# Kernel optimization log

Hardware: AMD Instinct MI355X
Metric: run time of the kernel (lower is better)

The kernel has to match this reference:

```python
import jax, jax.numpy as jnp
import numpy as np

B, T1, CHUNK = 4, 512, 64
LEFT, RIGHT = 256, 64
T2 = T1 + LEFT + RIGHT          # 832
NPOS = 2 * T1 - 1 + LEFT + RIGHT  # 1343
NFEAT, H, DK = 1024, 16, 64


def setup_inputs() -> dict:
    key = jax.random.key(0)
    ks = jax.random.split(key, 14)
    s = 0.02
    inp = {
        "query":   jax.random.normal(ks[0], (B, T1, NFEAT), jnp.float32),
        "key":     jax.random.normal(ks[1], (B, T2, NFEAT), jnp.float32),
        "value":   jax.random.normal(ks[2], (B, T2, NFEAT), jnp.float32),
        "pos_emb": jax.random.normal(ks[3], (1, NPOS, NFEAT), jnp.float32),
        "Wq":   jax.random.normal(ks[4], (NFEAT, NFEAT), jnp.float32) * s,
        "bq":   jax.random.normal(ks[5], (NFEAT,), jnp.float32) * s,
        "Wk":   jax.random.normal(ks[6], (NFEAT, NFEAT), jnp.float32) * s,
        "bk":   jax.random.normal(ks[7], (NFEAT,), jnp.float32) * s,
        "Wv":   jax.random.normal(ks[8], (NFEAT, NFEAT), jnp.float32) * s,
        "bv":   jax.random.normal(ks[9], (NFEAT,), jnp.float32) * s,
        "Wpos": jax.random.normal(ks[10], (NFEAT, NFEAT), jnp.float32) * s,
        "Wout": jax.random.normal(ks[11], (NFEAT, NFEAT), jnp.float32) * s,
        "bout": jax.random.normal(ks[12], (NFEAT,), jnp.float32) * s,
        "pos_bias_u": jax.random.normal(ks[13], (H, DK), jnp.float32) * s,
        "pos_bias_v": jax.random.normal(jax.random.fold_in(key, 99), (H, DK), jnp.float32) * s,
    }
    # chunk mask with right context: key index j maps to absolute position a = j - LEFT;
    # query i (chunk c = i // CHUNK) may attend a in [c*CHUNK - LEFT, (c+1)*CHUNK + RIGHT)
    c = np.arange(T1) // CHUNK
    a = np.arange(T2) - LEFT
    allowed = (a[None, :] < (c[:, None] + 1) * CHUNK + RIGHT) & (a[None, :] >= c[:, None] * CHUNK - LEFT)
    inp["mask"] = jnp.broadcast_to(jnp.asarray(allowed, dtype=bool)[None], (B, T1, T2))
    inp["left_context_size"] = LEFT
    inp["right_context_size"] = RIGHT
    return inp


def _rel_shift(x, left, right):
    # x: (b, h, t1, 2*t1-1+left+right) -> (b, h, t1, t1+left+right)
    # matches torch as_strided: out[..., i, j] = x[..., i, j - i + t1 - 1]
    b, h, t1, n = x.shape
    t2 = t1 + left + right
    idx = jnp.arange(t2)[None, :] - jnp.arange(t1)[:, None] + (t1 - 1)  # (t1, t2)
    return jnp.take_along_axis(x, idx[None, None], axis=-1)


def reference(query, key, value, pos_emb, mask, Wq, bq, Wk, bk, Wv, bv,
              Wpos, Wout, bout, pos_bias_u, pos_bias_v,
              left_context_size, right_context_size):
    b, t1, _ = query.shape
    q = (query @ Wq.T + bq).reshape(b, t1, H, DK)                       # (b, t1, h, d)
    k = (key @ Wk.T + bk).reshape(b, -1, H, DK).transpose(0, 2, 1, 3)    # (b, h, t2, d)
    v = (value @ Wv.T + bv).reshape(b, -1, H, DK).transpose(0, 2, 1, 3)  # (b, h, t2, d)
    p = (pos_emb @ Wpos.T).reshape(pos_emb.shape[0], -1, H, DK).transpose(0, 2, 1, 3)  # (1, h, n, d)

    q_u = (q + pos_bias_u).transpose(0, 2, 1, 3)   # (b, h, t1, d)
    q_v = (q + pos_bias_v).transpose(0, 2, 1, 3)   # (b, h, t1, d)

    matrix_ac = jnp.einsum('bhqd,bhkd->bhqk', q_u, k)          # (b, h, t1, t2)
    matrix_bd = jnp.einsum('bhqd,ohnd->bhqn', q_v, p)          # (b, h, t1, n)
    matrix_bd = _rel_shift(matrix_bd, left_context_size, right_context_size)

    scores = (matrix_ac + matrix_bd) / jnp.sqrt(jnp.float32(DK))
    m = mask[:, None, :, :]                                    # (b, 1, t1, t2), True = attend
    scores = jnp.where(m, scores, -jnp.inf)
    attn = jax.nn.softmax(scores.astype(jnp.float32), axis=-1).astype(value.dtype)
    attn = jnp.where(m, attn, 0.0)

    x = jnp.einsum('bhqk,bhkd->bqhd', attn, v).reshape(b, t1, H * DK)
    out = x @ Wout.T + bout                                     # (b, t1, n_feat)
    new_cache = jnp.concatenate([k, v], axis=-1)                # (b, h, t2, 2*d)
    return out, new_cache
```

## Files before the change

### kernel.cpp

```cpp
#include <hip/hip_runtime.h>
#include <cstdint>

typedef unsigned short u16;
using short8 = __attribute__((ext_vector_type(8))) short;
using f32x4  = __attribute__((ext_vector_type(4))) float;

#define T1 512
#define T2 832
#define NH 16
#define NPLOC 448

__device__ __forceinline__ u16 f2b(float f){
  union { float f; uint32_t u; } c; c.f = f;
  uint32_t u = c.u;
  u += 0x7fffu + ((u >> 16) & 1u);
  return (u16)(u >> 16);
}
__device__ __forceinline__ float b2f(u16 b){
  union { uint32_t u; float f; } c; c.u = (uint32_t)b << 16; return c.f;
}
__device__ __forceinline__ void async16(const void* g, void* l){
  __builtin_amdgcn_global_load_lds(
      (const __attribute__((address_space(1))) unsigned int*)g,
      (__attribute__((address_space(3))) unsigned int*)l, 16, 0, 0);
}

struct CvtSeg { const float* src; u16* dst; int nblk; };
struct CvtArgs { CvtSeg s[9]; };

__global__ __launch_bounds__(256) void cvt_all(CvtArgs a){
  int rel = blockIdx.x, seg = 0;
  while (rel >= a.s[seg].nblk){ rel -= a.s[seg].nblk; ++seg; }
  int i = rel * 256 + threadIdx.x;
  float4 v = ((const float4*)a.s[seg].src)[i];
  uint64_t p = (uint64_t)f2b(v.x) | ((uint64_t)f2b(v.y) << 16)
             | ((uint64_t)f2b(v.z) << 32) | ((uint64_t)f2b(v.w) << 48);
  *(uint64_t*)(a.s[seg].dst + (size_t)i * 4) = p;
}

__device__ __forceinline__ void gemm_core128(const u16* __restrict__ A, const u16* __restrict__ W,
    int m0, int n0, int tid, f32x4 acc[4][4])
{
  __shared__ __align__(16) u16 As0[4096];
  __shared__ __align__(16) u16 As1[4096];
  __shared__ __align__(16) u16 Bs0[4096];
  __shared__ __align__(16) u16 Bs1[4096];

  int lane = tid & 63, w = tid >> 6;
  int wr = w >> 1, wc = w & 1;
  const int lr = lane & 15, g = lane >> 4;
  const int sslot = (g ^ ((lr >> 1) & 3)) * 8;

  int r = tid >> 2;
  int ssl = ((tid & 3) ^ ((tid >> 3) & 3)) * 8;
  const u16* Asrc = A + (size_t)(m0 + r) * 1024 + ssl;
  const u16* Bsrc = W + (size_t)(n0 + r) * 1024 + ssl;

  auto stage = [&](int k0, u16* as, u16* bs){
    async16(Asrc + k0,         as + tid*8);
    async16(Asrc + 65536 + k0, as + 2048 + tid*8);
    async16(Bsrc + k0,         bs + tid*8);
    async16(Bsrc + 65536 + k0, bs + 2048 + tid*8);
  };

  auto step = [&](u16* as, u16* bs, int kstage, bool do_stage, bool last){
    if (last) asm volatile("s_waitcnt vmcnt(0)" ::: "memory");
    else      asm volatile("s_waitcnt vmcnt(4)" ::: "memory");
    __builtin_amdgcn_sched_barrier(0);
    __builtin_amdgcn_s_barrier();
    __builtin_amdgcn_sched_barrier(0);
    short8 a[4], b[4];
    #pragma unroll
    for (int m = 0; m < 4; ++m) a[m] = *(const short8*)&as[(wr*64 + m*16 + lr)*32 + sslot];
    #pragma unroll
    for (int n = 0; n < 4; ++n) b[n] = *(const short8*)&bs[(wc*64 + n*16 + lr)*32 + sslot];
    asm volatile("s_waitcnt lgkmcnt(0)" ::: "memory");
    __builtin_amdgcn_sched_barrier(0);
    __builtin_amdgcn_s_barrier();
    __builtin_amdgcn_sched_barrier(0);
    if (do_stage) stage(kstage, as, bs);
    __builtin_amdgcn_sched_barrier(0);
    __builtin_amdgcn_s_setprio(1);
    #pragma unroll
    for (int m = 0; m < 4; ++m)
      #pragma unroll
      for (int n = 0; n < 4; ++n)
        acc[m][n] = __builtin_amdgcn_mfma_f32_16x16x32_bf16(a[m], b[n], acc[m][n], 0, 0, 0);
    __builtin_amdgcn_s_setprio(0);
  };

  stage(0,  As0, Bs0);
  stage(32, As1, Bs1);
  __builtin_amdgcn_sched_barrier(0);
  for (int it = 0; it < 16; ++it){
    step(As0, Bs0, it*64 + 64, it < 15, false);
    step(As1, Bs1, it*64 + 96, it < 15, it == 15);
  }
}

__device__ __forceinline__ void gemm_core64(const u16* __restrict__ A, const u16* __restrict__ W,
    int m0, int n0, int tid, f32x4 acc[4][2])
{
  __shared__ __align__(16) u16 As0[2048];
  __shared__ __align__(16) u16 As1[2048];
  __shared__ __align__(16) u16 Bs0[4096];
  __shared__ __align__(16) u16 Bs1[4096];

  int lane = tid & 63, wc = tid >> 6;
  const int lr = lane & 15, g = lane >> 4;
  const int sslot = (g ^ ((lr >> 1) & 3)) * 8;

  int r = tid >> 2;
  int ssl = ((tid & 3) ^ ((tid >> 3) & 3)) * 8;
  const u16* Asrc = A + (size_t)(m0 + r) * 1024 + ssl;
  const u16* Bsrc = W + (size_t)(n0 + r) * 1024 + ssl;

  auto stage = [&](int k0, u16* as, u16* bs){
    async16(Asrc + k0,         as + tid*8);
    async16(Bsrc + k0,         bs + tid*8);
    async16(Bsrc + 65536 + k0, bs + 2048 + tid*8);
  };

  auto step = [&](u16* as, u16* bs, int kstage, bool do_stage, bool last){
    if (last) asm volatile("s_waitcnt vmcnt(0)" ::: "memory");
    else      asm volatile("s_waitcnt vmcnt(3)" ::: "memory");
    __builtin_amdgcn_sched_barrier(0);
    __builtin_amdgcn_s_barrier();
    __builtin_amdgcn_sched_barrier(0);
    short8 a[4], b[2];
    #pragma unroll
    for (int m = 0; m < 4; ++m) a[m] = *(const short8*)&as[(m*16 + lr)*32 + sslot];
    #pragma unroll
    for (int n = 0; n < 2; ++n) b[n] = *(const short8*)&bs[(wc*32 + n*16 + lr)*32 + sslot];
    asm volatile("s_waitcnt lgkmcnt(0)" ::: "memory");
    __builtin_amdgcn_sched_barrier(0);
    __builtin_amdgcn_s_barrier();
    __builtin_amdgcn_sched_barrier(0);
    if (do_stage) stage(kstage, as, bs);
    __builtin_amdgcn_sched_barrier(0);
    __builtin_amdgcn_s_setprio(1);
    #pragma unroll
    for (int m = 0; m < 4; ++m)
      #pragma unroll
      for (int n = 0; n < 2; ++n)
        acc[m][n] = __builtin_amdgcn_mfma_f32_16x16x32_bf16(a[m], b[n], acc[m][n], 0, 0, 0);
    __builtin_amdgcn_s_setprio(0);
  };

  stage(0,  As0, Bs0);
  stage(32, As1, Bs1);
  __builtin_amdgcn_sched_barrier(0);
  for (int it = 0; it < 16; ++it){
    step(As0, Bs0, it*64 + 64, it < 15, false);
    step(As1, Bs1, it*64 + 96, it < 15, it == 15);
  }
}

struct G4Args {
  const u16 *q, *k, *v, *p;
  const u16 *Wq, *Wk, *Wv, *Wp;
  const float *bq, *bk, *bv, *pbu, *pbv;
  u16 *qu, *qv2, *katt, *vatt, *patt;
  float *cache;
};

__global__ __launch_bounds__(256, 4) void gemm4(G4Args ga){
  int bid0 = blockIdx.x;
  int bid = (bid0 & 7) * 72 + (bid0 >> 3);
  int tid = threadIdx.x;
  int mode, mb; const u16 *A, *W;
  if (bid < 128)      { mode = 0; mb = bid >> 3;         A = ga.q; W = ga.Wq; }
  else if (bid < 336) { mode = 1; mb = (bid - 128) >> 3; A = ga.k; W = ga.Wk; }
  else if (bid < 544) { mode = 2; mb = (bid - 336) >> 3; A = ga.v; W = ga.Wv; }
  else                { mode = 3; mb = (bid - 544) >> 3; A = ga.p; W = ga.Wp; }
  int m0 = mb * 128, n0 = (bid & 7) * 128;
  f32x4 acc[4][4] = {};
  gemm_core128(A, W, m0, n0, tid, acc);

  int lane = tid & 63, w = tid >> 6;
  int wr = w >> 1, wc = w & 1;
  const int lr = lane & 15, g = lane >> 4;
  #pragma unroll
  for (int m = 0; m < 4; ++m){
    #pragma unroll
    for (int n = 0; n < 4; ++n){
      #pragma unroll
      for (int j = 0; j < 4; ++j){
        int row = m0 + wr*64 + m*16 + g*4 + j;
        int col = n0 + wc*64 + n*16 + lr;
        float vv = acc[m][n][j];
        if (mode == 0){
          vv += ga.bq[col];
          int h = col >> 6, d = col & 63, b_ = row >> 9, t = row & 511;
          size_t o = ((size_t)((b_*NH + h)*T1 + t))*64 + d;
          ga.qu [o] = f2b(vv + ga.pbu[col]);
          ga.qv2[o] = f2b(vv + ga.pbv[col]);
        } else if (mode == 1 || mode == 2){
          vv += (mode == 1 ? ga.bk : ga.bv)[col];
          int h = col >> 6, d = col & 63;
          int b_ = row / T2, t2 = row - b_*T2;
          size_t base = (size_t)(b_*NH + h)*T2 + t2;
          ga.cache[base*128 + (mode == 2 ? 64 : 0) + d] = vv;
          (mode == 1 ? ga.katt : ga.vatt)[base*64 + d] = f2b(vv);
        } else {
          if (row < NPLOC){
            int h = col >> 6, d = col & 63;
            ga.patt[((size_t)h*NPLOC + row)*64 + d] = f2b(vv);
          }
        }
      }
    }
  }
}

__global__ __launch_bounds__(256, 4) void gemm_out(const u16* __restrict__ A, const u16* __restrict__ W,
                                                   const float* __restrict__ bias, float* __restrict__ out){
  int bid0 = blockIdx.x;
  int bid = (bid0 & 7) * 32 + (bid0 >> 3);
  int m0 = (bid >> 3) * 64, n0 = (bid & 7) * 128;
  int tid = threadIdx.x;
  f32x4 acc[4][2] = {};
  gemm_core64(A, W, m0, n0, tid, acc);
  int lane = tid & 63, wc = tid >> 6;
  const int lr = lane & 15, g = lane >> 4;
  #pragma unroll
  for (int m = 0; m < 4; ++m)
    #pragma unroll
    for (int n = 0; n < 2; ++n)
      #pragma unroll
      for (int j = 0; j < 4; ++j){
        int row = m0 + m*16 + g*4 + j;
        int col = n0 + wc*32 + n*16 + lr;
        out[(size_t)row*1024 + col] = acc[m][n][j] + bias[col];
      }
}

#define PHASE_HEAD(N) \
  asm volatile("s_waitcnt vmcnt(" #N ")" ::: "memory"); \
  __builtin_amdgcn_sched_barrier(0); \
  __builtin_amdgcn_s_barrier(); \
  __builtin_amdgcn_sched_barrier(0);

#define PHASE_TAIL \
  __builtin_amdgcn_sched_barrier(0); \
  __builtin_amdgcn_s_barrier(); \
  __builtin_amdgcn_sched_barrier(0);

#define VT_TAIL \
  asm volatile("s_waitcnt lgkmcnt(0)" ::: "memory"); \
  __builtin_amdgcn_sched_barrier(0); \
  __builtin_amdgcn_s_barrier(); \
  __builtin_amdgcn_sched_barrier(0);

__global__ __launch_bounds__(256, 2) void attn_v3(
    const u16* __restrict__ qu, const u16* __restrict__ qv,
    const u16* __restrict__ katt, const u16* __restrict__ vatt,
    const u16* __restrict__ patt, u16* __restrict__ xout)
{
  __shared__ __align__(16) u16 SB[64*384];
  __shared__ __align__(16) u16 S0[8192];
  __shared__ __align__(16) u16 S1[8192];

  int tid = threadIdx.x, lane = tid & 63, w = tid >> 6;
  int bid0 = blockIdx.x;
  int bid = (bid0 & 7) * 64 + (bid0 >> 3);
  int c = bid & 7, h = (bid >> 3) & 15, b = bid >> 7;
  int bh = b*NH + h;
  const int lr = lane & 15, g = lane >> 4, lk = g * 8;

  auto sb_off = [&](int r, int cc) -> uint32_t {
    return ((uint32_t)(r*384 + cc)*2) ^ ((uint32_t)(r & 15) << 4);
  };
  auto stg_swz = [&](uint32_t o) -> uint32_t { return o ^ (((o >> 7) & 7u) << 4); };
  auto vt_off = [&](int d, int kk) -> uint32_t {
    return ((uint32_t)(d*128 + kk)*2) ^ ((uint32_t)(((d & 7) ^ ((d >> 3) & 7))) << 4);
  };

  int qrow = 16*w + lr;
  const u16* qub = qu + ((size_t)bh*T1 + c*64 + qrow)*64;
  const u16* qvb = qv + ((size_t)bh*T1 + c*64 + qrow)*64;
  short8 qu0 = *(const short8*)(qub + lk);
  short8 qu1 = *(const short8*)(qub + 32 + lk);
  short8 qv0 = *(const short8*)(qvb + lk);
  short8 qv1 = *(const short8*)(qvb + 32 + lk);
  __builtin_amdgcn_sched_barrier(0);

  const char* psrc = (const char*)(patt + (size_t)h*NPLOC*64);
  const char* ksrc = (const char*)(katt + ((size_t)bh*T2 + c*64)*64);
  const u16*  vsrc = vatt + ((size_t)bh*T2 + c*64)*64;

  auto issue4 = [&](const char* src, u16* dst){
    #pragma unroll
    for (int i = 0; i < 4; ++i){
      uint32_t o = (uint32_t)(i*256 + tid)*16;
      async16(src + stg_swz(o), (char*)dst + o);
    }
  };

  uint4 vstg0, vstg1, vstg2, vstg3;
  auto vload = [&](int vc){
    const u16* vb = vsrc + vc*8192;
    vstg0 = *(const uint4*)(vb + (0*256 + tid)*8);
    vstg1 = *(const uint4*)(vb + (1*256 + tid)*8);
    vstg2 = *(const uint4*)(vb + (2*256 + tid)*8);
    vstg3 = *(const uint4*)(vb + (3*256 + tid)*8);
  };
  auto vtwrite = [&](u16* sbuf){
    #pragma unroll
    for (int i = 0; i < 4; ++i){
      uint4 vv4 = (i == 0) ? vstg0 : (i == 1) ? vstg1 : (i == 2) ? vstg2 : vstg3;
      int e = (i*256 + tid)*8;
      int kk = e >> 6, d0 = e & 63;
      u16 uu[8] = { (u16)(vv4.x & 0xffff), (u16)(vv4.x >> 16), (u16)(vv4.y & 0xffff), (u16)(vv4.y >> 16),
                    (u16)(vv4.z & 0xffff), (u16)(vv4.z >> 16), (u16)(vv4.w & 0xffff), (u16)(vv4.w >> 16) };
      #pragma unroll
      for (int j = 0; j < 8; ++j)
        *(u16*)((char*)sbuf + vt_off(d0 + j, kk)) = uu[j];
    }
  };

  #define BD_CHUNK(PC, SBUF) \
    _Pragma("unroll") \
    for (int nt = 0; nt < 8; ++nt){ \
      uint32_t bo = (uint32_t)((nt*16 + lr)*64)*2; \
      short8 b0 = *(const short8*)((const char*)SBUF + stg_swz(bo + lk*2)); \
      short8 b1 = *(const short8*)((const char*)SBUF + stg_swz(bo + (32 + lk)*2)); \
      f32x4 acc = {0.f,0.f,0.f,0.f}; \
      __builtin_amdgcn_s_setprio(1); \
      acc = __builtin_amdgcn_mfma_f32_16x16x32_bf16(qv0, b0, acc, 0, 0, 0); \
      acc = __builtin_amdgcn_mfma_f32_16x16x32_bf16(qv1, b1, acc, 0, 0, 0); \
      __builtin_amdgcn_s_setprio(0); \
      int nl = (PC)*128 + nt*16 + lr; \
      _Pragma("unroll") \
      for (int j = 0; j < 4; ++j){ \
        int r = 16*w + g*4 + j; \
        int jj = nl + r - 63; \
        if (jj >= 0 && jj < 384) *(u16*)((char*)SB + sb_off(r, jj)) = f2b(acc[j]); \
      } \
    }

  #define AC_CHUNK(KC, SBUF) \
    _Pragma("unroll") \
    for (int nt = 0; nt < 8; ++nt){ \
      uint32_t bo = (uint32_t)((nt*16 + lr)*64)*2; \
      short8 b0 = *(const short8*)((const char*)SBUF + stg_swz(bo + lk*2)); \
      short8 b1 = *(const short8*)((const char*)SBUF + stg_swz(bo + (32 + lk)*2)); \
      __builtin_amdgcn_s_setprio(1); \
      accs[(KC)*8 + nt] = __builtin_amdgcn_mfma_f32_16x16x32_bf16(qu0, b0, accs[(KC)*8 + nt], 0, 0, 0); \
      accs[(KC)*8 + nt] = __builtin_amdgcn_mfma_f32_16x16x32_bf16(qu1, b1, accs[(KC)*8 + nt], 0, 0, 0); \
      __builtin_amdgcn_s_setprio(0); \
    }

  #define PV_CHUNK(VC, SBUF) \
    _Pragma("unroll") \
    for (int kt = 0; kt < 4; ++kt){ \
      short8 a = *(const short8*)((const char*)SB + sb_off(16*w + lr, (VC)*128 + kt*32 + lk)); \
      __builtin_amdgcn_s_setprio(1); \
      _Pragma("unroll") \
      for (int n = 0; n < 4; ++n){ \
        short8 bb = *(const short8*)((const char*)SBUF + vt_off(n*16 + lr, kt*32 + lk)); \
        acco[n] = __builtin_amdgcn_mfma_f32_16x16x32_bf16(a, bb, acco[n], 0, 0, 0); \
      } \
      __builtin_amdgcn_s_setprio(0); \
    }

  f32x4 accs[24];
  #pragma unroll
  for (int t = 0; t < 24; ++t) accs[t] = (f32x4){0.f,0.f,0.f,0.f};
  f32x4 acco[4] = {};

  issue4(psrc,          S0);
  issue4(psrc + 16384,  S1);

  PHASE_HEAD(4) BD_CHUNK(0, S0) PHASE_TAIL issue4(psrc + 32768, S0);
  PHASE_HEAD(4) BD_CHUNK(1, S1) PHASE_TAIL issue4(psrc + 49152, S1);
  PHASE_HEAD(4) BD_CHUNK(2, S0) PHASE_TAIL issue4(ksrc,         S0);
  PHASE_HEAD(4) BD_CHUNK(3, S1) PHASE_TAIL issue4(ksrc + 16384, S1);
  PHASE_HEAD(4) AC_CHUNK(0, S0) PHASE_TAIL issue4(ksrc + 32768, S0);
  PHASE_HEAD(4) AC_CHUNK(1, S1) PHASE_TAIL vload(0);
  PHASE_HEAD(4) AC_CHUNK(2, S0)

  #pragma unroll
  for (int t = 0; t < 24; ++t)
    #pragma unroll
    for (int j = 0; j < 4; ++j){
      int r = 16*w + g*4 + j, cc = t*16 + lr;
      accs[t][j] += b2f(*(const u16*)((const char*)SB + sb_off(r, cc)));
    }
  float mx[4] = {-1e30f,-1e30f,-1e30f,-1e30f};
  #pragma unroll
  for (int t = 0; t < 24; ++t)
    #pragma unroll
    for (int j = 0; j < 4; ++j) mx[j] = fmaxf(mx[j], accs[t][j]);
  #pragma unroll
  for (int j = 0; j < 4; ++j){
    mx[j] = fmaxf(mx[j], __shfl_xor(mx[j], 1));
    mx[j] = fmaxf(mx[j], __shfl_xor(mx[j], 2));
    mx[j] = fmaxf(mx[j], __shfl_xor(mx[j], 4));
    mx[j] = fmaxf(mx[j], __shfl_xor(mx[j], 8));
  }
  float sm[4] = {0.f,0.f,0.f,0.f};
  #pragma unroll
  for (int t = 0; t < 24; ++t)
    #pragma unroll
    for (int j = 0; j < 4; ++j){
      accs[t][j] = __expf((accs[t][j] - mx[j]) * 0.125f);
      sm[j] += accs[t][j];
    }
  #pragma unroll
  for (int j = 0; j < 4; ++j){
    sm[j] += __shfl_xor(sm[j], 1);
    sm[j] += __shfl_xor(sm[j], 2);
    sm[j] += __shfl_xor(sm[j], 4);
    sm[j] += __shfl_xor(sm[j], 8);
    sm[j] = 1.f / sm[j];
  }
  #pragma unroll
  for (int t = 0; t < 24; ++t)
    #pragma unroll
    for (int j = 0; j < 4; ++j){
      int r = 16*w + g*4 + j, cc = t*16 + lr;
      *(u16*)((char*)SB + sb_off(r, cc)) = f2b(accs[t][j] * sm[j]);
    }

  asm volatile("s_waitcnt vmcnt(0)" ::: "memory");
  __builtin_amdgcn_sched_barrier(0);
  vtwrite(S1);
  vload(1);
  VT_TAIL

  PV_CHUNK(0, S1)
  asm volatile("s_waitcnt vmcnt(0)" ::: "memory");
  __builtin_amdgcn_sched_barrier(0);
  vtwrite(S0);
  vload(2);
  VT_TAIL

  PV_CHUNK(1, S0)
  asm volatile("s_waitcnt vmcnt(0)" ::: "memory");
  __builtin_amdgcn_sched_barrier(0);
  vtwrite(S1);
  VT_TAIL

  PV_CHUNK(2, S1)

  #pragma unroll
  for (int n = 0; n < 4; ++n)
    #pragma unroll
    for (int j = 0; j < 4; ++j){
      int r = 16*w + g*4 + j;
      int t = c*64 + r, d = n*16 + lr;
      xout[((size_t)b*T1 + t)*1024 + h*64 + d] = f2b(acco[n][j]);
    }
}

extern "C" void kernel_launch(void* const* d_in, const int* in_sizes, int n_in,
                              void* d_out, int out_size, void* d_ws, size_t ws_size,
                              hipStream_t stream)
{
  const float* query = (const float*)d_in[0];
  const float* key   = (const float*)d_in[1];
  const float* value = (const float*)d_in[2];
  const float* pos   = (const float*)d_in[3];
  const float* Wq  = (const float*)d_in[4];
  const float* bq  = (const float*)d_in[5];
  const float* Wk  = (const float*)d_in[6];
  const float* bk  = (const float*)d_in[7];
  const float* Wv  = (const float*)d_in[8];
  const float* bv  = (const float*)d_in[9];
  const float* Wp  = (const float*)d_in[10];
  const float* Wo  = (const float*)d_in[11];
  const float* bo  = (const float*)d_in[12];
  const float* pbu = (const float*)d_in[13];
  const float* pbv = (const float*)d_in[14];

  float* out   = (float*)d_out;
  float* cache = out + 2097152;

  u16* ws     = (u16*)d_ws;
  u16* q_bf   = ws;
  u16* key_bf = ws + 2097152;
  u16* val_bf = ws + 5505024;
  u16* pos_bf = ws + 8912896;
  u16* Wq_bf  = ws + 9437184;
  u16* Wk_bf  = ws + 10485760;
  u16* Wv_bf  = ws + 11534336;
  u16* Wp_bf  = ws + 12582912;
  u16* Wo_bf  = ws + 13631488;
  u16* qu_bf  = ws + 14680064;
  u16* qv_bf  = ws + 16777216;
  u16* katt   = ws + 18874368;
  u16* vatt   = ws + 22282240;
  u16* patt   = ws + 25690112;
  u16* x_bf   = ws + 26148864;

  CvtArgs ca;
  ca.s[0] = { query,            q_bf,   2048 };
  ca.s[1] = { key,              key_bf, 3328 };
  ca.s[2] = { value,            val_bf, 3328 };
  ca.s[3] = { Wq,               Wq_bf,  1024 };
  ca.s[4] = { Wk,               Wk_bf,  1024 };
  ca.s[5] = { Wv,               Wv_bf,  1024 };
  ca.s[6] = { Wp,               Wp_bf,  1024 };
  ca.s[7] = { Wo,               Wo_bf,  1024 };
  ca.s[8] = { pos + 448*1024,   pos_bf, 448 };
  cvt_all<<<14272, 256, 0, stream>>>(ca);

  G4Args ga;
  ga.q = q_bf; ga.k = key_bf; ga.v = val_bf; ga.p = pos_bf;
  ga.Wq = Wq_bf; ga.Wk = Wk_bf; ga.Wv = Wv_bf; ga.Wp = Wp_bf;
  ga.bq = bq; ga.bk = bk; ga.bv = bv; ga.pbu = pbu; ga.pbv = pbv;
  ga.qu = qu_bf; ga.qv2 = qv_bf; ga.katt = katt; ga.vatt = vatt; ga.patt = patt;
  ga.cache = cache;
  gemm4<<<576, 256, 0, stream>>>(ga);

  attn_v3<<<512, 256, 0, stream>>>(qu_bf, qv_bf, katt, vatt, patt, x_bf);

  gemm_out<<<256, 256, 0, stream>>>(x_bf, Wo_bf, bo, out);
}
```

Measured before the change: 89.84 us.

## Fuse fp32-to-bf16 activation conversion into projection GEMM A-tile loads

The projection GEMM now reads the fp32 query/key/value/pos activations directly into registers, converts them to bf16 and writes them to LDS. This replaces the async global-to-LDS copies from a pre-converted buffer, so the separate conversion pass now only handles the weights. It removes the extra write and re-read of the bf16 activation buffers, but the GEMM loads twice as many bytes of A per tile, uses more registers (occupancy bound lowered from 4 to 3), and does conversion ALU work inside the main loop.

```diff
diff --git a/kernel.cpp b/kernel.cpp
--- a/kernel.cpp
+++ b/kernel.cpp
@@ -25,8 +25,10 @@
       (__attribute__((address_space(3))) unsigned int*)l, 16, 0, 0);
 }
 
+#define SB0 __builtin_amdgcn_sched_barrier(0)
+
 struct CvtSeg { const float* src; u16* dst; int nblk; };
-struct CvtArgs { CvtSeg s[9]; };
+struct CvtArgs { CvtSeg s[5]; };
 
 __global__ __launch_bounds__(256) void cvt_all(CvtArgs a){
   int rel = blockIdx.x, seg = 0;
@@ -38,148 +40,103 @@
   *(uint64_t*)(a.s[seg].dst + (size_t)i * 4) = p;
 }
 
-__device__ __forceinline__ void gemm_core128(const u16* __restrict__ A, const u16* __restrict__ W,
-    int m0, int n0, int tid, f32x4 acc[4][4])
-{
-  __shared__ __align__(16) u16 As0[4096];
-  __shared__ __align__(16) u16 As1[4096];
-  __shared__ __align__(16) u16 Bs0[4096];
-  __shared__ __align__(16) u16 Bs1[4096];
-
-  int lane = tid & 63, w = tid >> 6;
-  int wr = w >> 1, wc = w & 1;
-  const int lr = lane & 15, g = lane >> 4;
-  const int sslot = (g ^ ((lr >> 1) & 3)) * 8;
-
-  int r = tid >> 2;
-  int ssl = ((tid & 3) ^ ((tid >> 3) & 3)) * 8;
-  const u16* Asrc = A + (size_t)(m0 + r) * 1024 + ssl;
-  const u16* Bsrc = W + (size_t)(n0 + r) * 1024 + ssl;
-
-  auto stage = [&](int k0, u16* as, u16* bs){
-    async16(Asrc + k0,         as + tid*8);
-    async16(Asrc + 65536 + k0, as + 2048 + tid*8);
-    async16(Bsrc + k0,         bs + tid*8);
-    async16(Bsrc + 65536 + k0, bs + 2048 + tid*8);
-  };
-
-  auto step = [&](u16* as, u16* bs, int kstage, bool do_stage, bool last){
-    if (last) asm volatile("s_waitcnt vmcnt(0)" ::: "memory");
-    else      asm volatile("s_waitcnt vmcnt(4)" ::: "memory");
-    __builtin_amdgcn_sched_barrier(0);
-    __builtin_amdgcn_s_barrier();
-    __builtin_amdgcn_sched_barrier(0);
-    short8 a[4], b[4];
-    #pragma unroll
-    for (int m = 0; m < 4; ++m) a[m] = *(const short8*)&as[(wr*64 + m*16 + lr)*32 + sslot];
-    #pragma unroll
-    for (int n = 0; n < 4; ++n) b[n] = *(const short8*)&bs[(wc*64 + n*16 + lr)*32 + sslot];
-    asm volatile("s_waitcnt lgkmcnt(0)" ::: "memory");
-    __builtin_amdgcn_sched_barrier(0);
-    __builtin_amdgcn_s_barrier();
-    __builtin_amdgcn_sched_barrier(0);
-    if (do_stage) stage(kstage, as, bs);
-    __builtin_amdgcn_sched_barrier(0);
-    __builtin_amdgcn_s_setprio(1);
-    #pragma unroll
-    for (int m = 0; m < 4; ++m)
-      #pragma unroll
-      for (int n = 0; n < 4; ++n)
-        acc[m][n] = __builtin_amdgcn_mfma_f32_16x16x32_bf16(a[m], b[n], acc[m][n], 0, 0, 0);
-    __builtin_amdgcn_s_setprio(0);
-  };
-
-  stage(0,  As0, Bs0);
-  stage(32, As1, Bs1);
-  __builtin_amdgcn_sched_barrier(0);
-  for (int it = 0; it < 16; ++it){
-    step(As0, Bs0, it*64 + 64, it < 15, false);
-    step(As1, Bs1, it*64 + 96, it < 15, it == 15);
-  }
-}
-
-__device__ __forceinline__ void gemm_core64(const u16* __restrict__ A, const u16* __restrict__ W,
-    int m0, int n0, int tid, f32x4 acc[4][2])
-{
-  __shared__ __align__(16) u16 As0[2048];
-  __shared__ __align__(16) u16 As1[2048];
-  __shared__ __align__(16) u16 Bs0[4096];
-  __shared__ __align__(16) u16 Bs1[4096];
-
-  int lane = tid & 63, wc = tid >> 6;
-  const int lr = lane & 15, g = lane >> 4;
-  const int sslot = (g ^ ((lr >> 1) & 3)) * 8;
-
-  int r = tid >> 2;
-  int ssl = ((tid & 3) ^ ((tid >> 3) & 3)) * 8;
-  const u16* Asrc = A + (size_t)(m0 + r) * 1024 + ssl;
-  const u16* Bsrc = W + (size_t)(n0 + r) * 1024 + ssl;
-
-  auto stage = [&](int k0, u16* as, u16* bs){
-    async16(Asrc + k0,         as + tid*8);
-    async16(Bsrc + k0,         bs + tid*8);
-    async16(Bsrc + 65536 + k0, bs + 2048 + tid*8);
-  };
-
-  auto step = [&](u16* as, u16* bs, int kstage, bool do_stage, bool last){
-    if (last) asm volatile("s_waitcnt vmcnt(0)" ::: "memory");
-    else      asm volatile("s_waitcnt vmcnt(3)" ::: "memory");
-    __builtin_amdgcn_sched_barrier(0);
-    __builtin_amdgcn_s_barrier();
-    __builtin_amdgcn_sched_barrier(0);
-    short8 a[4], b[2];
-    #pragma unroll
-    for (int m = 0; m < 4; ++m) a[m] = *(const short8*)&as[(m*16 + lr)*32 + sslot];
-    #pragma unroll
-    for (int n = 0; n < 2; ++n) b[n] = *(const short8*)&bs[(wc*32 + n*16 + lr)*32 + sslot];
-    asm volatile("s_waitcnt lgkmcnt(0)" ::: "memory");
-    __builtin_amdgcn_sched_barrier(0);
-    __builtin_amdgcn_s_barrier();
-    __builtin_amdgcn_sched_barrier(0);
-    if (do_stage) stage(kstage, as, bs);
-    __builtin_amdgcn_sched_barrier(0);
-    __builtin_amdgcn_s_setprio(1);
-    #pragma unroll
-    for (int m = 0; m < 4; ++m)
-      #pragma unroll
-      for (int n = 0; n < 2; ++n)
-        acc[m][n] = __builtin_amdgcn_mfma_f32_16x16x32_bf16(a[m], b[n], acc[m][n], 0, 0, 0);
-    __builtin_amdgcn_s_setprio(0);
-  };
-
-  stage(0,  As0, Bs0);
-  stage(32, As1, Bs1);
-  __builtin_amdgcn_sched_barrier(0);
-  for (int it = 0; it < 16; ++it){
-    step(As0, Bs0, it*64 + 64, it < 15, false);
-    step(As1, Bs1, it*64 + 96, it < 15, it == 15);
-  }
-}
-
 struct G4Args {
-  const u16 *q, *k, *v, *p;
+  const float *q, *k, *v, *p;
   const u16 *Wq, *Wk, *Wv, *Wp;
   const float *bq, *bk, *bv, *pbu, *pbv;
   u16 *qu, *qv2, *katt, *vatt, *patt;
   float *cache;
 };
 
-__global__ __launch_bounds__(256, 4) void gemm4(G4Args ga){
+__global__ __launch_bounds__(256, 3) void gemm4(G4Args ga){
+  __shared__ __align__(16) u16 As0[4096];
+  __shared__ __align__(16) u16 As1[4096];
+  __shared__ __align__(16) u16 Bs0[4096];
+  __shared__ __align__(16) u16 Bs1[4096];
+
   int bid0 = blockIdx.x;
   int bid = (bid0 & 7) * 72 + (bid0 >> 3);
   int tid = threadIdx.x;
-  int mode, mb; const u16 *A, *W;
+  int mode, mb; const float *A; const u16 *W;
   if (bid < 128)      { mode = 0; mb = bid >> 3;         A = ga.q; W = ga.Wq; }
   else if (bid < 336) { mode = 1; mb = (bid - 128) >> 3; A = ga.k; W = ga.Wk; }
   else if (bid < 544) { mode = 2; mb = (bid - 336) >> 3; A = ga.v; W = ga.Wv; }
   else                { mode = 3; mb = (bid - 544) >> 3; A = ga.p; W = ga.Wp; }
   int m0 = mb * 128, n0 = (bid & 7) * 128;
-  f32x4 acc[4][4] = {};
-  gemm_core128(A, W, m0, n0, tid, acc);
 
   int lane = tid & 63, w = tid >> 6;
   int wr = w >> 1, wc = w & 1;
   const int lr = lane & 15, g = lane >> 4;
+  const int sslot = (g ^ ((lr >> 1) & 3)) * 8;
+
+  int r = tid >> 2;
+  int ssl = ((tid & 3) ^ ((tid >> 3) & 3)) * 8;
+  const float* Af  = A + (size_t)(m0 + r) * 1024 + ssl;
+  const u16*  Bsrc = W + (size_t)(n0 + r) * 1024 + ssl;
+
+  f32x4 acc[4][4] = {};
+  float4 xA0, xA1, xA2, xA3, yA0, yA1, yA2, yA3;
+
+#define LOADX(K) { xA0 = *(const float4*)(Af+(K)); xA1 = *(const float4*)(Af+(K)+4); \
+                   xA2 = *(const float4*)(Af+(K)+65536); xA3 = *(const float4*)(Af+(K)+65536+4); }
+#define LOADY(K) { yA0 = *(const float4*)(Af+(K)); yA1 = *(const float4*)(Af+(K)+4); \
+                   yA2 = *(const float4*)(Af+(K)+65536); yA3 = *(const float4*)(Af+(K)+65536+4); }
+#define WRX(AS) { short8 p0, p1; \
+  p0[0]=(short)f2b(xA0.x); p0[1]=(short)f2b(xA0.y); p0[2]=(short)f2b(xA0.z); p0[3]=(short)f2b(xA0.w); \
+  p0[4]=(short)f2b(xA1.x); p0[5]=(short)f2b(xA1.y); p0[6]=(short)f2b(xA1.z); p0[7]=(short)f2b(xA1.w); \
+  p1[0]=(short)f2b(xA2.x); p1[1]=(short)f2b(xA2.y); p1[2]=(short)f2b(xA2.z); p1[3]=(short)f2b(xA2.w); \
+  p1[4]=(short)f2b(xA3.x); p1[5]=(short)f2b(xA3.y); p1[6]=(short)f2b(xA3.z); p1[7]=(short)f2b(xA3.w); \
+  *(short8*)((AS) + tid*8) = p0; *(short8*)((AS) + 2048 + tid*8) = p1; }
+#define WRY(AS) { short8 p0, p1; \
+  p0[0]=(short)f2b(yA0.x); p0[1]=(short)f2b(yA0.y); p0[2]=(short)f2b(yA0.z); p0[3]=(short)f2b(yA0.w); \
+  p0[4]=(short)f2b(yA1.x); p0[5]=(short)f2b(yA1.y); p0[6]=(short)f2b(yA1.z); p0[7]=(short)f2b(yA1.w); \
+  p1[0]=(short)f2b(yA2.x); p1[1]=(short)f2b(yA2.y); p1[2]=(short)f2b(yA2.z); p1[3]=(short)f2b(yA2.w); \
+  p1[4]=(short)f2b(yA3.x); p1[5]=(short)f2b(yA3.y); p1[6]=(short)f2b(yA3.z); p1[7]=(short)f2b(yA3.w); \
+  *(short8*)((AS) + tid*8) = p0; *(short8*)((AS) + 2048 + tid*8) = p1; }
+#define ISSUEB(BS, K) { async16(Bsrc + (K), (BS) + tid*8); \
+                        async16(Bsrc + 65536 + (K), (BS) + 2048 + tid*8); }
+
+#define GSTEP(AS, BS, TOPW, DW, WRM, LDM, KA, KB, IA, IB) { \
+  asm volatile("s_waitcnt vmcnt(" #TOPW ")" ::: "memory"); \
+  SB0; __builtin_amdgcn_s_barrier(); SB0; \
+  short8 a_[4], b_[4]; \
+  _Pragma("unroll") \
+  for (int m = 0; m < 4; ++m) a_[m] = *(const short8*)&(AS)[(wr*64 + m*16 + lr)*32 + sslot]; \
+  _Pragma("unroll") \
+  for (int n = 0; n < 4; ++n) b_[n] = *(const short8*)&(BS)[(wc*64 + n*16 + lr)*32 + sslot]; \
+  asm volatile("s_waitcnt lgkmcnt(0)" ::: "memory"); \
+  SB0; __builtin_amdgcn_s_barrier(); SB0; \
+  if (DW){ asm volatile("s_waitcnt vmcnt(2)" ::: "memory"); SB0; WRM(AS); } \
+  if (IA){ LDM(KA); } \
+  if (IB){ ISSUEB(BS, KB); } \
+  SB0; \
+  __builtin_amdgcn_s_setprio(1); \
+  _Pragma("unroll") \
+  for (int m = 0; m < 4; ++m) \
+    _Pragma("unroll") \
+    for (int n = 0; n < 4; ++n) \
+      acc[m][n] = __builtin_amdgcn_mfma_f32_16x16x32_bf16(a_[m], b_[n], acc[m][n], 0, 0, 0); \
+  __builtin_amdgcn_s_setprio(0); }
+
+  LOADX(0);
+  ISSUEB(Bs0, 0);
+  LOADY(32);
+  asm volatile("s_waitcnt vmcnt(6)" ::: "memory"); SB0;
+  WRX(As0);
+  LOADX(64);
+  ISSUEB(Bs1, 32);
+  asm volatile("s_waitcnt vmcnt(6)" ::: "memory"); SB0;
+  WRY(As1);
+  asm volatile("s_waitcnt lgkmcnt(0)" ::: "memory"); SB0;
+
+  for (int it = 0; it < 15; ++it){
+    int t0 = 2*it;
+    GSTEP(As0, Bs0, 6, 1, WRX, LOADY, (t0+3)*32, (t0+2)*32, 1, 1)
+    GSTEP(As1, Bs1, 6, 1, WRY, LOADX, (t0+4)*32, (t0+3)*32, it < 14, 1)
+  }
+  GSTEP(As0, Bs0, 2, 0, WRX, LOADX, 0, 0, 0, 0)
+  GSTEP(As1, Bs1, 0, 0, WRX, LOADX, 0, 0, 0, 0)
+
   #pragma unroll
   for (int m = 0; m < 4; ++m){
     #pragma unroll
@@ -213,6 +170,60 @@
   }
 }
 
+__device__ __forceinline__ void gemm_core64(const u16* __restrict__ A, const u16* __restrict__ W,
+    int m0, int n0, int tid, f32x4 acc[4][2])
+{
+  __shared__ __align__(16) u16 As0[2048];
+  __shared__ __align__(16) u16 As1[2048];
+  __shared__ __align__(16) u16 Bs0[4096];
+  __shared__ __align__(16) u16 Bs1[4096];
+
+  int lane = tid & 63, wc = tid >> 6;
+  const int lr = lane & 15, g = lane >> 4;
+  const int sslot = (g ^ ((lr >> 1) & 3)) * 8;
+
+  int r = tid >> 2;
+  int ssl = ((tid & 3) ^ ((tid >> 3) & 3)) * 8;
+  const u16* Asrc = A + (size_t)(m0 + r) * 1024 + ssl;
+  const u16* Bsrc = W + (size_t)(n0 + r) * 1024 + ssl;
+
+  auto stage = [&](int k0, u16* as, u16* bs){
+    async16(Asrc + k0,         as + tid*8);
+    async16(Bsrc + k0,         bs + tid*8);
+    async16(Bsrc + 65536 + k0, bs + 2048 + tid*8);
+  };
+
+  auto step = [&](u16* as, u16* bs, int kstage, bool do_stage, bool last){
+    if (last) asm volatile("s_waitcnt vmcnt(0)" ::: "memory");
+    else      asm volatile("s_waitcnt vmcnt(3)" ::: "memory");
+    SB0; __builtin_amdgcn_s_barrier(); SB0;
+    short8 a[4], b[2];
+    #pragma unroll
+    for (int m = 0; m < 4; ++m) a[m] = *(const short8*)&as[(m*16 + lr)*32 + sslot];
+    #pragma unroll
+    for (int n = 0; n < 2; ++n) b[n] = *(const short8*)&bs[(wc*32 + n*16 + lr)*32 + sslot];
+    asm volatile("s_waitcnt lgkmcnt(0)" ::: "memory");
+    SB0; __builtin_amdgcn_s_barrier(); SB0;
+    if (do_stage) stage(kstage, as, bs);
+    SB0;
+    __builtin_amdgcn_s_setprio(1);
+    #pragma unroll
+    for (int m = 0; m < 4; ++m)
+      #pragma unroll
+      for (int n = 0; n < 2; ++n)
+        acc[m][n] = __builtin_amdgcn_mfma_f32_16x16x32_bf16(a[m], b[n], acc[m][n], 0, 0, 0);
+    __builtin_amdgcn_s_setprio(0);
+  };
+
+  stage(0,  As0, Bs0);
+  stage(32, As1, Bs1);
+  SB0;
+  for (int it = 0; it < 16; ++it){
+    step(As0, Bs0, it*64 + 64, it < 15, false);
+    step(As1, Bs1, it*64 + 96, it < 15, it == 15);
+  }
+}
+
 __global__ __launch_bounds__(256, 4) void gemm_out(const u16* __restrict__ A, const u16* __restrict__ W,
                                                    const float* __restrict__ bias, float* __restrict__ out){
   int bid0 = blockIdx.x;
@@ -237,20 +248,14 @@
 
 #define PHASE_HEAD(N) \
   asm volatile("s_waitcnt vmcnt(" #N ")" ::: "memory"); \
-  __builtin_amdgcn_sched_barrier(0); \
-  __builtin_amdgcn_s_barrier(); \
-  __builtin_amdgcn_sched_barrier(0);
+  SB0; __builtin_amdgcn_s_barrier(); SB0;
 
 #define PHASE_TAIL \
-  __builtin_amdgcn_sched_barrier(0); \
-  __builtin_amdgcn_s_barrier(); \
-  __builtin_amdgcn_sched_barrier(0);
+  SB0; __builtin_amdgcn_s_barrier(); SB0;
 
 #define VT_TAIL \
   asm volatile("s_waitcnt lgkmcnt(0)" ::: "memory"); \
-  __builtin_amdgcn_sched_barrier(0); \
-  __builtin_amdgcn_s_barrier(); \
-  __builtin_amdgcn_sched_barrier(0);
+  SB0; __builtin_amdgcn_s_barrier(); SB0;
 
 __global__ __launch_bounds__(256, 2) void attn_v3(
     const u16* __restrict__ qu, const u16* __restrict__ qv,
@@ -283,7 +288,7 @@
   short8 qu1 = *(const short8*)(qub + 32 + lk);
   short8 qv0 = *(const short8*)(qvb + lk);
   short8 qv1 = *(const short8*)(qvb + 32 + lk);
-  __builtin_amdgcn_sched_barrier(0);
+  SB0;
 
   const char* psrc = (const char*)(patt + (size_t)h*NPLOC*64);
   const char* ksrc = (const char*)(katt + ((size_t)bh*T2 + c*64)*64);
@@ -424,21 +429,21 @@
     }
 
   asm volatile("s_waitcnt vmcnt(0)" ::: "memory");
-  __builtin_amdgcn_sched_barrier(0);
+  SB0;
   vtwrite(S1);
   vload(1);
   VT_TAIL
 
   PV_CHUNK(0, S1)
   asm volatile("s_waitcnt vmcnt(0)" ::: "memory");
-  __builtin_amdgcn_sched_barrier(0);
+  SB0;
   vtwrite(S0);
   vload(2);
   VT_TAIL
 
   PV_CHUNK(1, S0)
   asm volatile("s_waitcnt vmcnt(0)" ::: "memory");
-  __builtin_amdgcn_sched_barrier(0);
+  SB0;
   vtwrite(S1);
   VT_TAIL
 
@@ -478,10 +483,6 @@
   float* cache = out + 2097152;
 
   u16* ws     = (u16*)d_ws;
-  u16* q_bf   = ws;
-  u16* key_bf = ws + 2097152;
-  u16* val_bf = ws + 5505024;
-  u16* pos_bf = ws + 8912896;
   u16* Wq_bf  = ws + 9437184;
   u16* Wk_bf  = ws + 10485760;
   u16* Wv_bf  = ws + 11534336;
@@ -495,19 +496,15 @@
   u16* x_bf   = ws + 26148864;
 
   CvtArgs ca;
-  ca.s[0] = { query,            q_bf,   2048 };
-  ca.s[1] = { key,              key_bf, 3328 };
-  ca.s[2] = { value,            val_bf, 3328 };
-  ca.s[3] = { Wq,               Wq_bf,  1024 };
-  ca.s[4] = { Wk,               Wk_bf,  1024 };
-  ca.s[5] = { Wv,               Wv_bf,  1024 };
-  ca.s[6] = { Wp,               Wp_bf,  1024 };
-  ca.s[7] = { Wo,               Wo_bf,  1024 };
-  ca.s[8] = { pos + 448*1024,   pos_bf, 448 };
-  cvt_all<<<14272, 256, 0, stream>>>(ca);
+  ca.s[0] = { Wq, Wq_bf, 1024 };
+  ca.s[1] = { Wk, Wk_bf, 1024 };
+  ca.s[2] = { Wv, Wv_bf, 1024 };
+  ca.s[3] = { Wp, Wp_bf, 1024 };
+  ca.s[4] = { Wo, Wo_bf, 1024 };
+  cvt_all<<<5120, 256, 0, stream>>>(ca);
 
   G4Args ga;
-  ga.q = q_bf; ga.k = key_bf; ga.v = val_bf; ga.p = pos_bf;
+  ga.q = query; ga.k = key; ga.v = value; ga.p = pos + 448*1024;
   ga.Wq = Wq_bf; ga.Wk = Wk_bf; ga.Wv = Wv_bf; ga.Wp = Wp_bf;
   ga.bq = bq; ga.bk = bk; ga.bv = bv; ga.pbu = pbu; ga.pbv = pbv;
   ga.qu = qu_bf; ga.qv2 = qv_bf; ga.katt = katt; ga.vatt = vatt; ga.patt = patt;
```

Result: no change. 89.51 us (-0.4%).
